# Kernel tuning notes

Measured on AMD Instinct MI355X. Metric: run time of the kernel, lower is better.

## Reference

```python
import jax, jax.numpy as jnp
import numpy as np

BATCH, SEQ, D_IN = 4, 2048, 1024
STATE, D_OUT, KX = 1024, 1024, 10


def setup_inputs() -> dict:
    key = jax.random.key(0)
    k0, k1, k2, k3, k4, k5 = jax.random.split(key, 6)
    inputs = jax.random.normal(k0, (BATCH, SEQ, D_IN), jnp.float32)
    h0 = jax.random.normal(k1, (STATE,), jnp.float32)
    A = jax.random.normal(k2, (STATE,), jnp.float32)
    A = A / jnp.max(jnp.abs(A))  # matches init_A / max|init_A|
    B = jax.random.normal(k3, (D_IN, STATE), jnp.float32) / D_IN
    C = jax.random.normal(k4, (STATE, D_OUT), jnp.float32) / STATE
    M = jax.random.normal(k5, (D_IN, D_OUT, KX), jnp.float32) / D_OUT
    return {"inputs": inputs, "h0": h0, "A": A, "B": B, "C": C, "M": M}


def compute_ar_x_preds(w, x):
    # w: (d_out, d_in, k); x: (b, l, d_in)
    d_out, d_in, k = w.shape
    b, l, _ = x.shape
    o = jnp.einsum('oik,bli->bklo', w, x)  # (b, k, l, d_out)
    shifts = jnp.arange(k)
    # roll slice i forward by i along the length axis
    o = jax.vmap(lambda oi, s: jnp.roll(oi, s, axis=1), in_axes=(1, 0), out_axes=1)(o, shifts)
    # triu mask: keep position t in slice i only if t >= i (causal AR)
    m = (jnp.arange(l)[None, :] >= shifts[:, None]).astype(o.dtype)  # (k, l)
    return jnp.sum(o * m[None, :, :, None], axis=1)  # (b, l, d_out)


def reference(inputs, h0, A, B, C, M):
    bsz = inputs.shape[0]
    h_init = jnp.broadcast_to(h0, (bsz, h0.shape[0]))  # h0.expand(bsz, state_dim)
    u_seq = jnp.swapaxes(inputs, 0, 1)  # (l, b, d_in)

    def step(h, u):
        h_new = A * h + u @ B  # diagonal recurrence
        return h_new, h_new

    _, hs = jax.lax.scan(step, h_init, u_seq)  # (l, b, state)
    all_h_t = jnp.swapaxes(hs, 0, 1)  # (b, l, state)
    lds_out = all_h_t @ C  # (b, l, d_out)
    ar = compute_ar_x_preds(M, inputs)
    return lds_out + ar
```

## Files before the change

kernel.cpp:

```cpp
#include <hip/hip_runtime.h>
#include <stdint.h>

typedef unsigned short u16;
typedef __attribute__((ext_vector_type(4))) float f32x4;
typedef __attribute__((ext_vector_type(8))) short s16x8;

#define BATCH 4
#define SEQ   2048
#define DIM   1024
#define KX    10
#define PAD   16
#define SEQP  (SEQ+PAD)

__device__ __forceinline__ u16 f2b(float f) {
    union { float f; uint32_t u; } v; v.f = f;
    uint32_t u = v.u + 0x7fffu + ((v.u >> 16) & 1u);
    return (u16)(u >> 16);
}
__device__ __forceinline__ float b2f(u16 h) {
    union { uint32_t u; float f; } v; v.u = ((uint32_t)h) << 16;
    return v.f;
}

__device__ __forceinline__ void llds16(const u16* g, u16* l) {
    __builtin_amdgcn_global_load_lds(
        (const __attribute__((address_space(1))) uint32_t*)g,
        (__attribute__((address_space(3))) uint32_t*)l, 16, 0, 0);
}

#define PREP_X_END  8256
#define PREP_B_END  9280
#define PREP_C_END  10304
#define PREP_M_END  14400

__global__ __launch_bounds__(256) void k_prep(
    const float* __restrict__ x, const float* __restrict__ B,
    const float* __restrict__ C, const float* __restrict__ M,
    u16* __restrict__ Xpad, u16* __restrict__ Btr, u16* __restrict__ Wall)
{
    __shared__ float tile[32][33];
    const int bid = blockIdx.x, tid = threadIdx.x;

    if (bid < PREP_X_END) {
        int idx = bid * 256 + tid;
        long e = (long)idx * 4;
        int i = (int)(e & 1023);
        int row = (int)(e >> 10);
        int t = row % SEQP;
        int b = row / SEQP;
        ushort4 o;
        if (t < PAD) {
            o.x = 0; o.y = 0; o.z = 0; o.w = 0;
        } else {
            const float4 v = *(const float4*)(x + (((long)(b * SEQ + (t - PAD)) << 10) + i));
            o.x = f2b(v.x); o.y = f2b(v.y); o.z = f2b(v.z); o.w = f2b(v.w);
        }
        *(ushort4*)(Xpad + ((long)row << 10) + i) = o;
    } else if (bid < PREP_C_END) {
        const int tb = bid - PREP_X_END;
        const float* in = (tb < 1024) ? B : C;
        u16* out = (tb < 1024) ? Btr : Wall;
        int lb = tb & 1023;
        int bx = lb & 31, by = lb >> 5;
        int tx = tid & 31, ty = tid >> 5;
#pragma unroll
        for (int j = 0; j < 4; j++)
            tile[ty + j * 8][tx] = in[(long)(by * 32 + ty + j * 8) * 1024 + bx * 32 + tx];
        __syncthreads();
#pragma unroll
        for (int j = 0; j < 4; j++)
            out[(long)(bx * 32 + ty + j * 8) * 1024 + by * 32 + tx] = f2b(tile[tx][ty + j * 8]);
    } else {
        int idx = (bid - PREP_C_END) * 256 + tid;
        int o = idx >> 10, i = idx & 1023;
        const float* src = M + (long)idx * KX;
#pragma unroll
        for (int k = 0; k < KX; k++)
            Wall[((long)(k + 1) << 20) + ((long)o << 10) + i] = f2b(src[k]);
    }
}


__global__ void k_scan1(const u16* __restrict__ U, const float* __restrict__ A,
                        float* __restrict__ F) {
    int s = blockIdx.x * 256 + threadIdx.x;
    int bc = blockIdx.y;
    int b = bc >> 4, c = bc & 15;
    float a = A[s];
    const u16* u = U + (((long)(b * SEQ + c * 128)) << 10) + s;
    float f = 0.f;
#pragma unroll 8
    for (int j = 0; j < 128; j++) f = fmaf(a, f, b2f(u[(long)j << 10]));
    F[((long)bc << 10) + s] = f;
}

__global__ void k_scan2(const float* __restrict__ F, const float* __restrict__ A,
                        const float* __restrict__ h0, float* __restrict__ Carry) {
    int idx = blockIdx.x * 256 + threadIdx.x;
    int b = idx >> 10, s = idx & 1023;
    float a = A[s];
    float a128 = a;
#pragma unroll
    for (int q = 0; q < 7; q++) a128 *= a128;
    float carry = h0[s];
#pragma unroll
    for (int c = 0; c < 16; c++) {
        long off = ((long)(b * 16 + c) << 10) + s;
        Carry[off] = carry;
        carry = fmaf(a128, carry, F[off]);
    }
}

__global__ void k_scan3(const u16* __restrict__ U, const float* __restrict__ A,
                        const float* __restrict__ Carry, u16* __restrict__ Hbf) {
    int s = blockIdx.x * 256 + threadIdx.x;
    int bc = blockIdx.y;
    int b = bc >> 4, c = bc & 15;
    float a = A[s];
    long base = (((long)(b * SEQ + c * 128)) << 10) + s;
    float h = Carry[((long)bc << 10) + s];
#pragma unroll 8
    for (int j = 0; j < 128; j++) {
        h = fmaf(a, h, b2f(U[base + ((long)j << 10)]));
        Hbf[base + ((long)j << 10)] = f2b(h);
    }
}

__global__ __launch_bounds__(256) void k_gemm(
    void* __restrict__ outv, const u16* __restrict__ Xpad,
    const u16* __restrict__ Hbf, const u16* __restrict__ W,
    int ngroups, int use_h, int bf16_out)
{
    __shared__ u16 At[128 * 64];
    __shared__ u16 Bt[128 * 64];

    const int tid  = threadIdx.x;
    const int wave = tid >> 6, lane = tid & 63;
    const int wm = wave >> 1, wn = wave & 1;
    const int quad = lane >> 4, l15 = lane & 15, l7 = lane & 7;

    const int col0 = blockIdx.x * 128;
    const int row0 = blockIdx.y * 128;
    const int b = row0 >> 11;
    const long Xrow0 = (long)b * SEQP + PAD + (row0 & (SEQ - 1));

    const int s_base = wave * 256 + lane;

    f32x4 acc[4][4];
#pragma unroll
    for (int i = 0; i < 4; i++)
#pragma unroll
        for (int j = 0; j < 4; j++)
            acc[i][j] = (f32x4){0.f, 0.f, 0.f, 0.f};

    for (int g = 0; g < ngroups; g++) {
        const u16* Ab;
        if (use_h && g == 0) {
            Ab = Hbf + ((long)row0 << 10);
        } else {
            int lag = use_h ? (g - 1) : 0;
            Ab = Xpad + ((Xrow0 - lag) << 10);
        }
        const u16* Wb = W + ((long)g << 20) + ((long)col0 << 10);

        for (int k0 = 0; k0 < 1024; k0 += 64) {
#pragma unroll
            for (int q = 0; q < 4; q++) {
                int s = s_base + q * 64;
                int row = s >> 3;
                int kc = (s & 7) ^ (row & 7);
                const u16* gA = Ab + ((long)row << 10) + k0 + kc * 8;
                const u16* gB = Wb + ((long)row << 10) + k0 + kc * 8;
                llds16(gA, &At[(wave * 256 + q * 64) * 8]);
                llds16(gB, &Bt[(wave * 256 + q * 64) * 8]);
            }
            __syncthreads();

            s16x8 af[4][2], bfr[4][2];
#pragma unroll
            for (int mi = 0; mi < 4; mi++) {
#pragma unroll
                for (int kk = 0; kk < 2; kk++) {
                    int kcu = ((kk * 4 + quad) ^ l7) << 3;
                    af[mi][kk]  = *(const s16x8*)&At[(wm * 64 + mi * 16 + l15) * 64 + kcu];
                    bfr[mi][kk] = *(const s16x8*)&Bt[(wn * 64 + mi * 16 + l15) * 64 + kcu];
                }
            }
#pragma unroll
            for (int mi = 0; mi < 4; mi++)
#pragma unroll
                for (int ni = 0; ni < 4; ni++) {
                    acc[mi][ni] = __builtin_amdgcn_mfma_f32_16x16x32_bf16(
                        af[mi][0], bfr[ni][0], acc[mi][ni], 0, 0, 0);
                    acc[mi][ni] = __builtin_amdgcn_mfma_f32_16x16x32_bf16(
                        af[mi][1], bfr[ni][1], acc[mi][ni], 0, 0, 0);
                }
            __syncthreads();
        }
    }

#pragma unroll
    for (int mi = 0; mi < 4; mi++) {
        int r = row0 + wm * 64 + mi * 16 + quad * 4;
#pragma unroll
        for (int ni = 0; ni < 4; ni++) {
            int c = col0 + wn * 64 + ni * 16 + l15;
            f32x4 v = acc[mi][ni];
            if (bf16_out) {
                u16* ob = (u16*)outv;
#pragma unroll
                for (int reg = 0; reg < 4; reg++)
                    ob[((long)(r + reg) << 10) + c] = f2b(v[reg]);
            } else {
                float* of = (float*)outv;
#pragma unroll
                for (int reg = 0; reg < 4; reg++)
                    of[((long)(r + reg) << 10) + c] = v[reg];
            }
        }
    }
}


extern "C" void kernel_launch(void* const* d_in, const int* in_sizes, int n_in,
                              void* d_out, int out_size, void* d_ws, size_t ws_size,
                              hipStream_t stream) {
    const float* x  = (const float*)d_in[0];
    const float* h0 = (const float*)d_in[1];
    const float* A  = (const float*)d_in[2];
    const float* B  = (const float*)d_in[3];
    const float* C  = (const float*)d_in[4];
    const float* M  = (const float*)d_in[5];
    float* out = (float*)d_out;

    char* ws = (char*)d_ws;
    u16*   Xpad  = (u16*)  (ws);
    u16*   Hbf   = (u16*)  (ws + 16908288);
    u16*   Wall  = (u16*)  (ws + 33685504);
    u16*   Btr   = (u16*)  (ws + 56754176);
    u16*   Ubf   = (u16*)  (ws + 58851328);
    float* F     = (float*)(ws + 75628544);
    float* Carry = (float*)(ws + 75890688);

    k_prep<<<dim3(PREP_M_END), dim3(256), 0, stream>>>(x, B, C, M, Xpad, Btr, Wall);

    k_gemm<<<dim3(8, 64), dim3(256), 0, stream>>>(Ubf, Xpad, Xpad, Btr, 1, 0, 1);

    k_scan1<<<dim3(4, 64), dim3(256), 0, stream>>>(Ubf, A, F);
    k_scan2<<<dim3(16), dim3(256), 0, stream>>>(F, A, h0, Carry);
    k_scan3<<<dim3(4, 64), dim3(256), 0, stream>>>(Ubf, A, Carry, Hbf);

    k_gemm<<<dim3(8, 64), dim3(256), 0, stream>>>(out, Xpad, Hbf, Wall, 11, 1, 0);
}
```

Before: 367.2 us.

## Share one X slab across lagged AR groups and double-buffer weight tiles

The GEMM now loads a 144-row slab of padded X once per k-step and reuses it for all ten lagged AR groups by offsetting the row index, instead of reloading a 128-row A tile for every group. Weight tiles are double-buffered and the next group's tile is prefetched while the current group's MFMAs run. The H group is handled last and overwrites the slab, and scan3 writes H in place over U, which frees a workspace buffer. This cuts global and LDS traffic for the A operand, at the cost of more LDS, reordered k/group loops and more complex swizzle indexing.

New measurement: 337.0 us. -8.2%, faster.

```diff
diff --git a/kernel.cpp b/kernel.cpp
--- a/kernel.cpp
+++ b/kernel.cpp
@@ -29,7 +29,6 @@
 }
 
 #define PREP_X_END  8256
-#define PREP_B_END  9280
 #define PREP_C_END  10304
 #define PREP_M_END  14400
 
@@ -111,8 +110,8 @@
     }
 }
 
-__global__ void k_scan3(const u16* __restrict__ U, const float* __restrict__ A,
-                        const float* __restrict__ Carry, u16* __restrict__ Hbf) {
+__global__ void k_scan3(u16* __restrict__ U, const float* __restrict__ A,
+                        const float* __restrict__ Carry) {
     int s = blockIdx.x * 256 + threadIdx.x;
     int bc = blockIdx.y;
     int b = bc >> 4, c = bc & 15;
@@ -122,7 +121,7 @@
 #pragma unroll 8
     for (int j = 0; j < 128; j++) {
         h = fmaf(a, h, b2f(U[base + ((long)j << 10)]));
-        Hbf[base + ((long)j << 10)] = f2b(h);
+        U[base + ((long)j << 10)] = f2b(h);
     }
 }
 
@@ -131,8 +130,8 @@
     const u16* __restrict__ Hbf, const u16* __restrict__ W,
     int ngroups, int use_h, int bf16_out)
 {
-    __shared__ u16 At[128 * 64];
-    __shared__ u16 Bt[128 * 64];
+    __shared__ u16 Asl[160 * 64];
+    __shared__ u16 Wb2[2][128 * 64];
 
     const int tid  = threadIdx.x;
     const int wave = tid >> 6, lane = tid & 63;
@@ -141,10 +140,10 @@
 
     const int col0 = blockIdx.x * 128;
     const int row0 = blockIdx.y * 128;
-    const int b = row0 >> 11;
-    const long Xrow0 = (long)b * SEQP + PAD + (row0 & (SEQ - 1));
-
-    const int s_base = wave * 256 + lane;
+    const int bb = row0 >> 11;
+    const long Xrow0 = (long)bb * SEQP + PAD + (row0 & (SEQ - 1));
+    const long XslabBase = (Xrow0 - 16) << 10;
+    const int lastg = ngroups - 1;
 
     f32x4 acc[4][4];
 #pragma unroll
@@ -153,37 +152,72 @@
         for (int j = 0; j < 4; j++)
             acc[i][j] = (f32x4){0.f, 0.f, 0.f, 0.f};
 
-    for (int g = 0; g < ngroups; g++) {
-        const u16* Ab;
-        if (use_h && g == 0) {
-            Ab = Hbf + ((long)row0 << 10);
-        } else {
-            int lag = use_h ? (g - 1) : 0;
-            Ab = Xpad + ((Xrow0 - lag) << 10);
-        }
-        const u16* Wb = W + ((long)g << 20) + ((long)col0 << 10);
-
-        for (int k0 = 0; k0 < 1024; k0 += 64) {
+    for (int k0 = 0; k0 < 1024; k0 += 64) {
+#pragma unroll
+        for (int q = 0; q < 5; q++) {
+            int u = wave * 320 + q * 64 + lane;
+            int row = u >> 3;
+            int kc = (u & 7) ^ (row & 7);
+            llds16(Xpad + XslabBase + ((long)row << 10) + k0 + kc * 8,
+                   &Asl[(wave * 320 + q * 64) * 8]);
+        }
+        {
+            int wsel = use_h ? 1 : 0;
+            const u16* Wg = W + ((long)wsel << 20) + ((long)col0 << 10);
 #pragma unroll
             for (int q = 0; q < 4; q++) {
-                int s = s_base + q * 64;
-                int row = s >> 3;
-                int kc = (s & 7) ^ (row & 7);
-                const u16* gA = Ab + ((long)row << 10) + k0 + kc * 8;
-                const u16* gB = Wb + ((long)row << 10) + k0 + kc * 8;
-                llds16(gA, &At[(wave * 256 + q * 64) * 8]);
-                llds16(gB, &Bt[(wave * 256 + q * 64) * 8]);
-            }
-            __syncthreads();
+                int u = wave * 256 + q * 64 + lane;
+                int row = u >> 3;
+                int kc = (u & 7) ^ (row & 7);
+                llds16(Wg + ((long)row << 10) + k0 + kc * 8,
+                       &Wb2[0][(wave * 256 + q * 64) * 8]);
+            }
+        }
+        __syncthreads();
+
+        for (int g = 0; g < ngroups; g++) {
+            const bool isH = use_h && (g == lastg);
+            if (isH) {
+                const u16* Hb = Hbf + ((long)row0 << 10);
+#pragma unroll
+                for (int q = 0; q < 4; q++) {
+                    int u = wave * 256 + q * 64 + lane;
+                    int row = u >> 3;
+                    int kc = (u & 7) ^ (row & 7);
+                    llds16(Hb + ((long)row << 10) + k0 + kc * 8,
+                           &Asl[(wave * 256 + q * 64) * 8]);
+                }
+                __syncthreads();
+            }
+            if (g < lastg) {
+                int gn = g + 1;
+                int wsel = use_h ? ((gn == lastg) ? 0 : gn + 1) : gn;
+                const u16* Wg = W + ((long)wsel << 20) + ((long)col0 << 10);
+                u16* dst = Wb2[gn & 1];
+#pragma unroll
+                for (int q = 0; q < 4; q++) {
+                    int u = wave * 256 + q * 64 + lane;
+                    int row = u >> 3;
+                    int kc = (u & 7) ^ (row & 7);
+                    llds16(Wg + ((long)row << 10) + k0 + kc * 8,
+                           &dst[(wave * 256 + q * 64) * 8]);
+                }
+            }
+
+            const int rbase = isH ? 0 : (16 - g);
+            const int r7 = (l15 + rbase) & 7;
+            const u16* Wrd = Wb2[g & 1];
 
             s16x8 af[4][2], bfr[4][2];
 #pragma unroll
             for (int mi = 0; mi < 4; mi++) {
+                int arow = rbase + wm * 64 + mi * 16 + l15;
 #pragma unroll
                 for (int kk = 0; kk < 2; kk++) {
-                    int kcu = ((kk * 4 + quad) ^ l7) << 3;
-                    af[mi][kk]  = *(const s16x8*)&At[(wm * 64 + mi * 16 + l15) * 64 + kcu];
-                    bfr[mi][kk] = *(const s16x8*)&Bt[(wn * 64 + mi * 16 + l15) * 64 + kcu];
+                    int kca = ((kk * 4 + quad) ^ r7) << 3;
+                    int kcb = ((kk * 4 + quad) ^ l7) << 3;
+                    af[mi][kk]  = *(const s16x8*)&Asl[arow * 64 + kca];
+                    bfr[mi][kk] = *(const s16x8*)&Wrd[(wn * 64 + mi * 16 + l15) * 64 + kcb];
                 }
             }
 #pragma unroll
@@ -235,20 +269,19 @@
 
     char* ws = (char*)d_ws;
     u16*   Xpad  = (u16*)  (ws);
-    u16*   Hbf   = (u16*)  (ws + 16908288);
-    u16*   Wall  = (u16*)  (ws + 33685504);
-    u16*   Btr   = (u16*)  (ws + 56754176);
-    u16*   Ubf   = (u16*)  (ws + 58851328);
-    float* F     = (float*)(ws + 75628544);
-    float* Carry = (float*)(ws + 75890688);
+    u16*   Wall  = (u16*)  (ws + 16908288);
+    u16*   Btr   = (u16*)  (ws + 39976960);
+    u16*   Ubf   = (u16*)  (ws + 42074112);
+    float* F     = (float*)(ws + 58851328);
+    float* Carry = (float*)(ws + 59113472);
 
     k_prep<<<dim3(PREP_M_END), dim3(256), 0, stream>>>(x, B, C, M, Xpad, Btr, Wall);
 
-    k_gemm<<<dim3(8, 64), dim3(256), 0, stream>>>(Ubf, Xpad, Xpad, Btr, 1, 0, 1);
+    k_gemm<<<dim3(8, 64), dim3(256), 0, stream>>>(Ubf, Xpad, Ubf, Btr, 1, 0, 1);
 
     k_scan1<<<dim3(4, 64), dim3(256), 0, stream>>>(Ubf, A, F);
     k_scan2<<<dim3(16), dim3(256), 0, stream>>>(F, A, h0, Carry);
-    k_scan3<<<dim3(4, 64), dim3(256), 0, stream>>>(Ubf, A, Carry, Hbf);
-
-    k_gemm<<<dim3(8, 64), dim3(256), 0, stream>>>(out, Xpad, Hbf, Wall, 11, 1, 0);
-}
+    k_scan3<<<dim3(4, 64), dim3(256), 0, stream>>>(Ubf, A, Carry);
+
+    k_gemm<<<dim3(8, 64), dim3(256), 0, stream>>>(out, Xpad, Ubf, Wall, 11, 1, 0);
+}
```
